# Kernel tuning notes

Hardware: AMD Instinct MI355X
Metric: run time of the kernel (lower is better)

The kernel has to match this reference:

```python
import jax, jax.numpy as jnp
import numpy as np

NUM_LEAVES = 256
EPS = 1e-6
SHARPNESS = 1.0   # init_sharpness, non-trainable buffer
BIAS_SHIFT = -2.0


def _generalized_gcd(w1, w2, lambd):
    # lambd: per-node bias -> andness via sigmoid; broadcast over batch
    lam = jax.nn.sigmoid(lambd)
    a = jnp.abs(w1) + EPS
    b = jnp.abs(w2) + EPS
    return lam * jnp.minimum(a, b) + (1.0 - lam) * jnp.maximum(a, b)


def setup_inputs() -> dict:
    key = jax.random.key(0)
    ks = jax.random.split(key, 6)
    B, L = 65536, NUM_LEAVES
    x = jax.random.normal(ks[0], (B, L), jnp.float32)
    # xavier-like scale for the leaf projection
    W_leaf = jax.random.normal(ks[1], (L, L), jnp.float32) * (1.0 / np.sqrt(L))
    weights = jax.random.uniform(ks[2], (L - 1, 2), jnp.float32, 0.5, 1.5)
    biases = jax.random.uniform(ks[3], (L - 1,), jnp.float32) * 0.1
    w_out = jax.random.normal(ks[4], (1, 1), jnp.float32)
    b_out = jnp.full((1,), 0.5, jnp.float32)
    return {"x": x, "W_leaf": W_leaf, "weights": weights,
            "biases": biases, "w_out": w_out, "b_out": b_out}


def reference(x, W_leaf, weights, biases, w_out, b_out):
    # InputToLeafFC: sigmoid(sharpness * (x @ W^T + bias_shift))
    leaf = jax.nn.sigmoid(SHARPNESS * (x @ W_leaf.T + BIAS_SHIFT))  # (B, L)

    # The original pops two nodes from the front of the queue and appends the
    # result; for a power-of-two leaf count this is exactly a level-by-level
    # pairwise tree reduction, with node weights consumed in order.
    cur = leaf
    off = 0
    n = cur.shape[1]
    while n > 1:  # log2(L) levels, each fully vectorized over (batch, pairs)
        m = n // 2
        w = weights[off:off + m]   # (m, 2)
        b = biases[off:off + m]    # (m,)
        left = cur[:, 0::2] * w[:, 0]
        right = cur[:, 1::2] * w[:, 1]
        cur = _generalized_gcd(left, right, b)  # (B, m)
        off += m
        n = m
    # fc_out: Linear(1,1) then sigmoid -> (B, 1)
    return jax.nn.sigmoid(cur * w_out[0, 0] + b_out[0])
```

## Files before the change

### kernel.cpp

```cpp
#include <hip/hip_runtime.h>
#include <stdint.h>


#define EPS 1e-6f
#define LOG2E 1.44269504088896340736f
#define WSTR 264
#define WIMG_SHORTS (256 * WSTR)
#define PARAM_OFF_B (WIMG_SHORTS * 2)

typedef __attribute__((ext_vector_type(8))) short short8;
typedef __attribute__((ext_vector_type(4))) short short4_t;
typedef __attribute__((ext_vector_type(4))) float float4_t;

__device__ __forceinline__ float fast_sigmoid(float z) {
    float e = __builtin_amdgcn_exp2f(-z * LOG2E);
    return __builtin_amdgcn_rcpf(1.0f + e);
}

__device__ __forceinline__ short f2bf(float f) {
    uint32_t u = __builtin_bit_cast(uint32_t, f);
    u += 0x7FFFu + ((u >> 16) & 1u);
    return (short)(u >> 16);
}

__device__ __forceinline__ float ggcd(float l, float r, float lam) {
    float a = fabsf(l) + EPS;
    float b = fabsf(r) + EPS;
    float mn = fminf(a, b);
    float mx = fmaxf(a, b);
    return fmaf(lam, mn - mx, mx);
}

__global__ __launch_bounds__(256)
void convert_w_kernel(const float* __restrict__ Wl,
                      const float* __restrict__ wts, const float* __restrict__ bia,
                      short* __restrict__ img) {
    int t = blockIdx.x * 256 + threadIdx.x;
    int j   = t >> 6;
    int kc4 = t & 63;
    const float4* Wv4 = (const float4*)Wl;
    float4 w4 = Wv4[j * 64 + kc4];
    int p = ((j & 15) << 4) | (j >> 4);
    short4_t s4;
    s4.x = f2bf(w4.x); s4.y = f2bf(w4.y); s4.z = f2bf(w4.z); s4.w = f2bf(w4.w);
    *(short4_t*)&img[p * WSTR + kc4 * 4] = s4;

    if (blockIdx.x == 0) {
        float4* pv = (float4*)((char*)img + PARAM_OFF_B);
        if (threadIdx.x < 255) {
            int n = threadIdx.x;
            pv[n] = make_float4(wts[2 * n], wts[2 * n + 1], fast_sigmoid(bia[n]), 0.f);
        } else if (threadIdx.x == 255) {
            pv[255] = make_float4(0.f, 0.f, 0.f, 0.f);
        }
    }
}

__global__ __launch_bounds__(1024, 4)
void btln_main(const float* __restrict__ x, const short* __restrict__ img,
               const float* __restrict__ wout, const float* __restrict__ bout,
               float* __restrict__ out) {
    __shared__ short Ws[WIMG_SHORTS];
    __shared__ float4 pv[256];

    const int tid  = threadIdx.x;
    const int lane = tid & 63;
    const int wv   = tid >> 6;
    const int c0   = lane & 15;
    const int q    = lane >> 4;

    {
        const uint4* img4 = (const uint4*)img;
        uint4* ws4 = (uint4*)Ws;
        const int n16 = (WIMG_SHORTS * 2) / 16;
        #pragma unroll
        for (int it = 0; it < 9; ++it) {
            int i = it * 1024 + tid;
            if (i < n16) ws4[i] = img4[i];
        }
        if (tid < 256) {
            const float4* gpv = (const float4*)((const char*)img + PARAM_OFF_B);
            pv[tid] = gpv[tid];
        }
    }
    __syncthreads();

    const int group   = blockIdx.x * 16 + wv;
    const int rowbase = group * 16;
    const float4* xv  = (const float4*)(x + (size_t)(rowbase + c0) * 256);

    float4_t acc[16];
    #pragma unroll
    for (int t = 0; t < 16; ++t) acc[t] = (float4_t){0.f, 0.f, 0.f, 0.f};

    float4 a0 = xv[q * 2];
    float4 a1 = xv[q * 2 + 1];
    #pragma unroll 1
    for (int kt = 0; kt < 8; ++kt) {
        const int ktn = (kt < 7) ? kt + 1 : 7;
        float4 b0 = xv[ktn * 8 + q * 2];
        float4 b1 = xv[ktn * 8 + q * 2 + 1];

        short8 af;
        af[0] = f2bf(a0.x); af[1] = f2bf(a0.y); af[2] = f2bf(a0.z); af[3] = f2bf(a0.w);
        af[4] = f2bf(a1.x); af[5] = f2bf(a1.y); af[6] = f2bf(a1.z); af[7] = f2bf(a1.w);

        const int kk = kt * 32;
        #pragma unroll
        for (int t = 0; t < 16; ++t) {
            short8 bf = *(const short8*)&Ws[(t * 16 + c0) * WSTR + kk + q * 8];
            acc[t] = __builtin_amdgcn_mfma_f32_16x16x32_bf16(af, bf, acc[t], 0, 0, 0);
        }
        a0 = b0; a1 = b1;
    }

    #pragma unroll
    for (int t = 0; t < 16; ++t) {
        #pragma unroll
        for (int r = 0; r < 4; ++r) acc[t][r] = fast_sigmoid(acc[t][r] - 2.0f);
    }
    #pragma unroll
    for (int tp = 0; tp < 8; ++tp) {
        float4 p = pv[c0 * 8 + tp];
        #pragma unroll
        for (int r = 0; r < 4; ++r)
            acc[tp][r] = ggcd(acc[2*tp][r] * p.x, acc[2*tp+1][r] * p.y, p.z);
    }
    #pragma unroll
    for (int tp = 0; tp < 4; ++tp) {
        float4 p = pv[128 + c0 * 4 + tp];
        #pragma unroll
        for (int r = 0; r < 4; ++r)
            acc[tp][r] = ggcd(acc[2*tp][r] * p.x, acc[2*tp+1][r] * p.y, p.z);
    }
    #pragma unroll
    for (int tp = 0; tp < 2; ++tp) {
        float4 p = pv[192 + c0 * 2 + tp];
        #pragma unroll
        for (int r = 0; r < 4; ++r)
            acc[tp][r] = ggcd(acc[2*tp][r] * p.x, acc[2*tp+1][r] * p.y, p.z);
    }
    float res[4];
    {
        float4 p = pv[224 + c0];
        #pragma unroll
        for (int r = 0; r < 4; ++r)
            res[r] = ggcd(acc[0][r] * p.x, acc[1][r] * p.y, p.z);
    }

    const int offs[4] = {240, 248, 252, 254};
    #pragma unroll
    for (int k = 0; k < 4; ++k) {
        float4 p = pv[offs[k] + (c0 >> (k + 1))];
        bool isLeft = ((c0 >> k) & 1) == 0;
        #pragma unroll
        for (int r = 0; r < 4; ++r) {
            float other = __shfl_xor(res[r], 1 << k, 64);
            float lf = isLeft ? res[r] : other;
            float rt = isLeft ? other  : res[r];
            res[r] = ggcd(lf * p.x, rt * p.y, p.z);
        }
    }

    if (c0 == 0) {
        const float wo = wout[0];
        const float bo = bout[0];
        #pragma unroll
        for (int r = 0; r < 4; ++r)
            out[rowbase + q * 4 + r] = fast_sigmoid(fmaf(res[r], wo, bo));
    }
}

extern "C" void kernel_launch(void* const* d_in, const int* in_sizes, int n_in,
                              void* d_out, int out_size, void* d_ws, size_t ws_size,
                              hipStream_t stream) {
    const float* x   = (const float*)d_in[0];
    const float* Wl  = (const float*)d_in[1];
    const float* wts = (const float*)d_in[2];
    const float* bia = (const float*)d_in[3];
    const float* wo  = (const float*)d_in[4];
    const float* bo  = (const float*)d_in[5];
    float* out = (float*)d_out;
    short* img = (short*)d_ws;

    convert_w_kernel<<<dim3(64), dim3(256), 0, stream>>>(Wl, wts, bia, img);

    const int rows = out_size;
    dim3 grid(rows / 256), block(1024);
    btln_main<<<grid, block, 0, stream>>>(x, img, wo, bo, out);
}
```

Baseline: 115.4 us.

## Fuse weight conversion into main kernel and process two row tiles per wave

Removes the separate W/param conversion kernel: each block now converts the fp32 W_leaf to bf16 straight into shared memory and computes the sigmoid biases itself. Blocks shrink to 512 threads, and each wave handles 32 rows as two 16-row MFMA tiles that share every B-fragment LDS read. This saves one launch and halves LDS traffic per MFMA, at the cost of redundant per-block conversion of W, more accumulator registers (two sets of 16 float4), and possibly lower occupancy.

```diff
diff --git a/kernel.cpp b/kernel.cpp
--- a/kernel.cpp
+++ b/kernel.cpp
@@ -6,7 +6,6 @@
 #define LOG2E 1.44269504088896340736f
 #define WSTR 264
 #define WIMG_SHORTS (256 * WSTR)
-#define PARAM_OFF_B (WIMG_SHORTS * 2)
 
 typedef __attribute__((ext_vector_type(8))) short short8;
 typedef __attribute__((ext_vector_type(4))) short short4_t;
@@ -31,89 +30,8 @@
     return fmaf(lam, mn - mx, mx);
 }
 
-__global__ __launch_bounds__(256)
-void convert_w_kernel(const float* __restrict__ Wl,
-                      const float* __restrict__ wts, const float* __restrict__ bia,
-                      short* __restrict__ img) {
-    int t = blockIdx.x * 256 + threadIdx.x;
-    int j   = t >> 6;
-    int kc4 = t & 63;
-    const float4* Wv4 = (const float4*)Wl;
-    float4 w4 = Wv4[j * 64 + kc4];
-    int p = ((j & 15) << 4) | (j >> 4);
-    short4_t s4;
-    s4.x = f2bf(w4.x); s4.y = f2bf(w4.y); s4.z = f2bf(w4.z); s4.w = f2bf(w4.w);
-    *(short4_t*)&img[p * WSTR + kc4 * 4] = s4;
-
-    if (blockIdx.x == 0) {
-        float4* pv = (float4*)((char*)img + PARAM_OFF_B);
-        if (threadIdx.x < 255) {
-            int n = threadIdx.x;
-            pv[n] = make_float4(wts[2 * n], wts[2 * n + 1], fast_sigmoid(bia[n]), 0.f);
-        } else if (threadIdx.x == 255) {
-            pv[255] = make_float4(0.f, 0.f, 0.f, 0.f);
-        }
-    }
-}
-
-__global__ __launch_bounds__(1024, 4)
-void btln_main(const float* __restrict__ x, const short* __restrict__ img,
-               const float* __restrict__ wout, const float* __restrict__ bout,
-               float* __restrict__ out) {
-    __shared__ short Ws[WIMG_SHORTS];
-    __shared__ float4 pv[256];
-
-    const int tid  = threadIdx.x;
-    const int lane = tid & 63;
-    const int wv   = tid >> 6;
-    const int c0   = lane & 15;
-    const int q    = lane >> 4;
-
-    {
-        const uint4* img4 = (const uint4*)img;
-        uint4* ws4 = (uint4*)Ws;
-        const int n16 = (WIMG_SHORTS * 2) / 16;
-        #pragma unroll
-        for (int it = 0; it < 9; ++it) {
-            int i = it * 1024 + tid;
-            if (i < n16) ws4[i] = img4[i];
-        }
-        if (tid < 256) {
-            const float4* gpv = (const float4*)((const char*)img + PARAM_OFF_B);
-            pv[tid] = gpv[tid];
-        }
-    }
-    __syncthreads();
-
-    const int group   = blockIdx.x * 16 + wv;
-    const int rowbase = group * 16;
-    const float4* xv  = (const float4*)(x + (size_t)(rowbase + c0) * 256);
-
-    float4_t acc[16];
-    #pragma unroll
-    for (int t = 0; t < 16; ++t) acc[t] = (float4_t){0.f, 0.f, 0.f, 0.f};
-
-    float4 a0 = xv[q * 2];
-    float4 a1 = xv[q * 2 + 1];
-    #pragma unroll 1
-    for (int kt = 0; kt < 8; ++kt) {
-        const int ktn = (kt < 7) ? kt + 1 : 7;
-        float4 b0 = xv[ktn * 8 + q * 2];
-        float4 b1 = xv[ktn * 8 + q * 2 + 1];
-
-        short8 af;
-        af[0] = f2bf(a0.x); af[1] = f2bf(a0.y); af[2] = f2bf(a0.z); af[3] = f2bf(a0.w);
-        af[4] = f2bf(a1.x); af[5] = f2bf(a1.y); af[6] = f2bf(a1.z); af[7] = f2bf(a1.w);
-
-        const int kk = kt * 32;
-        #pragma unroll
-        for (int t = 0; t < 16; ++t) {
-            short8 bf = *(const short8*)&Ws[(t * 16 + c0) * WSTR + kk + q * 8];
-            acc[t] = __builtin_amdgcn_mfma_f32_16x16x32_bf16(af, bf, acc[t], 0, 0, 0);
-        }
-        a0 = b0; a1 = b1;
-    }
-
+__device__ __forceinline__ void tree_reduce(float4_t acc[16], int c0,
+                                            const float4* pv, float res[4]) {
     #pragma unroll
     for (int t = 0; t < 16; ++t) {
         #pragma unroll
@@ -140,13 +58,84 @@
         for (int r = 0; r < 4; ++r)
             acc[tp][r] = ggcd(acc[2*tp][r] * p.x, acc[2*tp+1][r] * p.y, p.z);
     }
-    float res[4];
     {
         float4 p = pv[224 + c0];
         #pragma unroll
         for (int r = 0; r < 4; ++r)
             res[r] = ggcd(acc[0][r] * p.x, acc[1][r] * p.y, p.z);
     }
+}
+
+__global__ __launch_bounds__(512, 2)
+void btln_fused(const float* __restrict__ x, const float* __restrict__ Wl,
+                const float* __restrict__ wts, const float* __restrict__ bia,
+                const float* __restrict__ wout, const float* __restrict__ bout,
+                float* __restrict__ out) {
+    __shared__ short Ws[WIMG_SHORTS];
+    __shared__ float4 pv[256];
+
+    const int tid  = threadIdx.x;
+    const int lane = tid & 63;
+    const int wv   = tid >> 6;
+    const int c0   = lane & 15;
+    const int q    = lane >> 4;
+
+    {
+        const float4* Wv4 = (const float4*)Wl;
+        #pragma unroll 4
+        for (int it = 0; it < 32; ++it) {
+            int i   = it * 512 + tid;
+            int j   = i >> 6;
+            int kc4 = i & 63;
+            float4 w4 = Wv4[i];
+            int p = ((j & 15) << 4) | (j >> 4);
+            short4_t s4;
+            s4.x = f2bf(w4.x); s4.y = f2bf(w4.y); s4.z = f2bf(w4.z); s4.w = f2bf(w4.w);
+            *(short4_t*)&Ws[p * WSTR + kc4 * 4] = s4;
+        }
+    }
+    if (tid < 255)
+        pv[tid] = make_float4(wts[2 * tid], wts[2 * tid + 1], fast_sigmoid(bia[tid]), 0.f);
+    __syncthreads();
+
+    const int rowbase = blockIdx.x * 256 + wv * 32;
+    const float4* xv0 = (const float4*)(x + (size_t)(rowbase + c0) * 256);
+    const float4* xv1 = (const float4*)(x + (size_t)(rowbase + 16 + c0) * 256);
+
+    float4_t acc0[16], acc1[16];
+    #pragma unroll
+    for (int t = 0; t < 16; ++t) {
+        acc0[t] = (float4_t){0.f, 0.f, 0.f, 0.f};
+        acc1[t] = (float4_t){0.f, 0.f, 0.f, 0.f};
+    }
+
+    float4 a00 = xv0[q * 2], a01 = xv0[q * 2 + 1];
+    float4 a10 = xv1[q * 2], a11 = xv1[q * 2 + 1];
+    #pragma unroll 1
+    for (int kt = 0; kt < 8; ++kt) {
+        const int ktn = (kt < 7) ? kt + 1 : 7;
+        float4 n00 = xv0[ktn * 8 + q * 2], n01 = xv0[ktn * 8 + q * 2 + 1];
+        float4 n10 = xv1[ktn * 8 + q * 2], n11 = xv1[ktn * 8 + q * 2 + 1];
+
+        short8 af0, af1;
+        af0[0] = f2bf(a00.x); af0[1] = f2bf(a00.y); af0[2] = f2bf(a00.z); af0[3] = f2bf(a00.w);
+        af0[4] = f2bf(a01.x); af0[5] = f2bf(a01.y); af0[6] = f2bf(a01.z); af0[7] = f2bf(a01.w);
+        af1[0] = f2bf(a10.x); af1[1] = f2bf(a10.y); af1[2] = f2bf(a10.z); af1[3] = f2bf(a10.w);
+        af1[4] = f2bf(a11.x); af1[5] = f2bf(a11.y); af1[6] = f2bf(a11.z); af1[7] = f2bf(a11.w);
+
+        const int kk = kt * 32;
+        #pragma unroll
+        for (int t = 0; t < 16; ++t) {
+            short8 bf = *(const short8*)&Ws[(t * 16 + c0) * WSTR + kk + q * 8];
+            acc0[t] = __builtin_amdgcn_mfma_f32_16x16x32_bf16(af0, bf, acc0[t], 0, 0, 0);
+            acc1[t] = __builtin_amdgcn_mfma_f32_16x16x32_bf16(af1, bf, acc1[t], 0, 0, 0);
+        }
+        a00 = n00; a01 = n01; a10 = n10; a11 = n11;
+    }
+
+    float res0[4], res1[4];
+    tree_reduce(acc0, c0, pv, res0);
+    tree_reduce(acc1, c0, pv, res1);
 
     const int offs[4] = {240, 248, 252, 254};
     #pragma unroll
@@ -155,10 +144,12 @@
         bool isLeft = ((c0 >> k) & 1) == 0;
         #pragma unroll
         for (int r = 0; r < 4; ++r) {
-            float other = __shfl_xor(res[r], 1 << k, 64);
-            float lf = isLeft ? res[r] : other;
-            float rt = isLeft ? other  : res[r];
-            res[r] = ggcd(lf * p.x, rt * p.y, p.z);
+            float o0 = __shfl_xor(res0[r], 1 << k, 64);
+            float o1 = __shfl_xor(res1[r], 1 << k, 64);
+            float lf0 = isLeft ? res0[r] : o0, rt0 = isLeft ? o0 : res0[r];
+            float lf1 = isLeft ? res1[r] : o1, rt1 = isLeft ? o1 : res1[r];
+            res0[r] = ggcd(lf0 * p.x, rt0 * p.y, p.z);
+            res1[r] = ggcd(lf1 * p.x, rt1 * p.y, p.z);
         }
     }
 
@@ -166,8 +157,10 @@
         const float wo = wout[0];
         const float bo = bout[0];
         #pragma unroll
-        for (int r = 0; r < 4; ++r)
-            out[rowbase + q * 4 + r] = fast_sigmoid(fmaf(res[r], wo, bo));
+        for (int r = 0; r < 4; ++r) {
+            out[rowbase + q * 4 + r]      = fast_sigmoid(fmaf(res0[r], wo, bo));
+            out[rowbase + 16 + q * 4 + r] = fast_sigmoid(fmaf(res1[r], wo, bo));
+        }
     }
 }
 
@@ -181,11 +174,8 @@
     const float* wo  = (const float*)d_in[4];
     const float* bo  = (const float*)d_in[5];
     float* out = (float*)d_out;
-    short* img = (short*)d_ws;
-
-    convert_w_kernel<<<dim3(64), dim3(256), 0, stream>>>(Wl, wts, bia, img);
 
     const int rows = out_size;
-    dim3 grid(rows / 256), block(1024);
-    btln_main<<<grid, block, 0, stream>>>(x, img, wo, bo, out);
+    dim3 grid(rows / 256), block(512);
+    btln_fused<<<grid, block, 0, stream>>>(x, Wl, wts, bia, wo, bo, out);
 }
```

New measurement: 115.7 us. About the same (+0.3%).

## Stream swizzled bf16 weight tiles into double-buffered LDS via async global_load_lds

Applied to the files above, without the earlier changes.

The up-front copy of the full padded 135KB weight image into LDS is replaced by a K-tiled, XOR-swizzled weight layout. Each 64-wide K slab is streamed into a double-buffered 64KB LDS region with direct global-to-LDS loads, overlapped with the MFMA work on the previous slab. Blocks shrink to 512 threads and 128 rows to cut LDS use per block and allow more resident blocks. The cost is a barrier per K step and more blocks each re-reading the weight image from L2.

```diff
diff --git a/kernel.cpp b/kernel.cpp
--- a/kernel.cpp
+++ b/kernel.cpp
@@ -4,9 +4,7 @@
 
 #define EPS 1e-6f
 #define LOG2E 1.44269504088896340736f
-#define WSTR 264
-#define WIMG_SHORTS (256 * WSTR)
-#define PARAM_OFF_B (WIMG_SHORTS * 2)
+#define PARAM_OFF 131072
 
 typedef __attribute__((ext_vector_type(8))) short short8;
 typedef __attribute__((ext_vector_type(4))) short short4_t;
@@ -21,6 +19,13 @@
     uint32_t u = __builtin_bit_cast(uint32_t, f);
     u += 0x7FFFu + ((u >> 16) & 1u);
     return (short)(u >> 16);
+}
+
+__device__ __forceinline__ short8 pack8(float4 a, float4 b) {
+    short8 s;
+    s[0] = f2bf(a.x); s[1] = f2bf(a.y); s[2] = f2bf(a.z); s[3] = f2bf(a.w);
+    s[4] = f2bf(b.x); s[5] = f2bf(b.y); s[6] = f2bf(b.z); s[7] = f2bf(b.w);
+    return s;
 }
 
 __device__ __forceinline__ float ggcd(float l, float r, float lam) {
@@ -31,36 +36,80 @@
     return fmaf(lam, mn - mx, mx);
 }
 
+__device__ __forceinline__ void lds16(const void* g, void* l) {
+    __builtin_amdgcn_global_load_lds(
+        (const __attribute__((address_space(1))) unsigned int*)g,
+        (__attribute__((address_space(3))) unsigned int*)l, 16, 0, 0);
+}
+
+__device__ __forceinline__ void tree_reduce(float4_t acc[16], int c0,
+                                            const float4* pv, float res[4]) {
+    #pragma unroll
+    for (int t = 0; t < 16; ++t) {
+        #pragma unroll
+        for (int r = 0; r < 4; ++r) acc[t][r] = fast_sigmoid(acc[t][r] - 2.0f);
+    }
+    #pragma unroll
+    for (int tp = 0; tp < 8; ++tp) {
+        float4 p = pv[c0 * 8 + tp];
+        #pragma unroll
+        for (int r = 0; r < 4; ++r)
+            acc[tp][r] = ggcd(acc[2*tp][r] * p.x, acc[2*tp+1][r] * p.y, p.z);
+    }
+    #pragma unroll
+    for (int tp = 0; tp < 4; ++tp) {
+        float4 p = pv[128 + c0 * 4 + tp];
+        #pragma unroll
+        for (int r = 0; r < 4; ++r)
+            acc[tp][r] = ggcd(acc[2*tp][r] * p.x, acc[2*tp+1][r] * p.y, p.z);
+    }
+    #pragma unroll
+    for (int tp = 0; tp < 2; ++tp) {
+        float4 p = pv[192 + c0 * 2 + tp];
+        #pragma unroll
+        for (int r = 0; r < 4; ++r)
+            acc[tp][r] = ggcd(acc[2*tp][r] * p.x, acc[2*tp+1][r] * p.y, p.z);
+    }
+    {
+        float4 p = pv[224 + c0];
+        #pragma unroll
+        for (int r = 0; r < 4; ++r)
+            res[r] = ggcd(acc[0][r] * p.x, acc[1][r] * p.y, p.z);
+    }
+}
+
 __global__ __launch_bounds__(256)
-void convert_w_kernel(const float* __restrict__ Wl,
-                      const float* __restrict__ wts, const float* __restrict__ bia,
-                      short* __restrict__ img) {
-    int t = blockIdx.x * 256 + threadIdx.x;
-    int j   = t >> 6;
-    int kc4 = t & 63;
-    const float4* Wv4 = (const float4*)Wl;
-    float4 w4 = Wv4[j * 64 + kc4];
-    int p = ((j & 15) << 4) | (j >> 4);
+void convert_w(const float* __restrict__ Wl, const float* __restrict__ wts,
+               const float* __restrict__ bia, char* __restrict__ img) {
+    int i = blockIdx.x * 256 + threadIdx.x;
+    int a = i * 8;
+    int kt   = a >> 15;
+    int s    = a & 32767;
+    int j    = s >> 7;
+    int b    = s & 127;
+    int cpos = b >> 4;
+    int h    = (b >> 3) & 1;
+    int c    = cpos ^ (j & 7);
+    int k    = kt * 64 + c * 8 + h * 4;
+    int src  = ((j & 15) << 4) | (j >> 4);
+    float4 w4 = *(const float4*)&Wl[src * 256 + k];
     short4_t s4;
     s4.x = f2bf(w4.x); s4.y = f2bf(w4.y); s4.z = f2bf(w4.z); s4.w = f2bf(w4.w);
-    *(short4_t*)&img[p * WSTR + kc4 * 4] = s4;
-
-    if (blockIdx.x == 0) {
-        float4* pv = (float4*)((char*)img + PARAM_OFF_B);
-        if (threadIdx.x < 255) {
-            int n = threadIdx.x;
-            pv[n] = make_float4(wts[2 * n], wts[2 * n + 1], fast_sigmoid(bia[n]), 0.f);
-        } else if (threadIdx.x == 255) {
-            pv[255] = make_float4(0.f, 0.f, 0.f, 0.f);
-        }
-    }
-}
-
-__global__ __launch_bounds__(1024, 4)
-void btln_main(const float* __restrict__ x, const short* __restrict__ img,
+    *(short4_t*)&img[a] = s4;
+
+    if (i < 255) {
+        float4* pv = (float4*)(img + PARAM_OFF);
+        pv[i] = make_float4(wts[2 * i], wts[2 * i + 1], fast_sigmoid(bia[i]), 0.f);
+    } else if (i == 255) {
+        ((float4*)(img + PARAM_OFF))[255] = make_float4(0.f, 0.f, 0.f, 0.f);
+    }
+}
+
+__global__ __launch_bounds__(512, 4)
+void btln_main(const float* __restrict__ x, const char* __restrict__ img,
                const float* __restrict__ wout, const float* __restrict__ bout,
                float* __restrict__ out) {
-    __shared__ short Ws[WIMG_SHORTS];
+    __shared__ short Wt[2][16384];
     __shared__ float4 pv[256];
 
     const int tid  = threadIdx.x;
@@ -69,84 +118,63 @@
     const int c0   = lane & 15;
     const int q    = lane >> 4;
 
+    if (tid < 256) pv[tid] = ((const float4*)(img + PARAM_OFF))[tid];
+
     {
-        const uint4* img4 = (const uint4*)img;
-        uint4* ws4 = (uint4*)Ws;
-        const int n16 = (WIMG_SHORTS * 2) / 16;
-        #pragma unroll
-        for (int it = 0; it < 9; ++it) {
-            int i = it * 1024 + tid;
-            if (i < n16) ws4[i] = img4[i];
+        const char* g = img + wv * 4096 + lane * 16;
+        char* l = (char*)&Wt[0][wv * 2048];
+        #pragma unroll
+        for (int it = 0; it < 4; ++it)
+            lds16(g + it * 1024, l + it * 1024);
+    }
+
+    const int rowbase = blockIdx.x * 128 + wv * 16;
+    const float* xr = x + (size_t)(rowbase + c0) * 256;
+
+    float4_t acc[16];
+    #pragma unroll
+    for (int t = 0; t < 16; ++t) acc[t] = (float4_t){0.f, 0.f, 0.f, 0.f};
+
+    float4 a0 = *(const float4*)(xr + q * 8);
+    float4 a1 = *(const float4*)(xr + q * 8 + 4);
+    float4 a2 = *(const float4*)(xr + 32 + q * 8);
+    float4 a3 = *(const float4*)(xr + 32 + q * 8 + 4);
+
+    __syncthreads();
+
+    const int vx = c0 & 7;
+    #pragma unroll 1
+    for (int kt = 0; kt < 4; ++kt) {
+        const short* cur = Wt[kt & 1];
+        if (kt < 3) {
+            const char* g = img + (kt + 1) * 32768 + wv * 4096 + lane * 16;
+            char* l = (char*)&Wt[(kt + 1) & 1][wv * 2048];
+            #pragma unroll
+            for (int it = 0; it < 4; ++it)
+                lds16(g + it * 1024, l + it * 1024);
         }
-        if (tid < 256) {
-            const float4* gpv = (const float4*)((const char*)img + PARAM_OFF_B);
-            pv[tid] = gpv[tid];
+        const int kn = (kt < 3 ? kt + 1 : 3) * 64;
+        float4 b0 = *(const float4*)(xr + kn + q * 8);
+        float4 b1 = *(const float4*)(xr + kn + q * 8 + 4);
+        float4 b2 = *(const float4*)(xr + kn + 32 + q * 8);
+        float4 b3 = *(const float4*)(xr + kn + 32 + q * 8 + 4);
+
+        short8 af0 = pack8(a0, a1);
+        short8 af1 = pack8(a2, a3);
+        #pragma unroll
+        for (int t = 0; t < 16; ++t) {
+            const short* base = &cur[(t * 16 + c0) * 64];
+            short8 bf0 = *(const short8*)&base[(q ^ vx) * 8];
+            short8 bf1 = *(const short8*)&base[((q + 4) ^ vx) * 8];
+            acc[t] = __builtin_amdgcn_mfma_f32_16x16x32_bf16(af0, bf0, acc[t], 0, 0, 0);
+            acc[t] = __builtin_amdgcn_mfma_f32_16x16x32_bf16(af1, bf1, acc[t], 0, 0, 0);
         }
-    }
-    __syncthreads();
-
-    const int group   = blockIdx.x * 16 + wv;
-    const int rowbase = group * 16;
-    const float4* xv  = (const float4*)(x + (size_t)(rowbase + c0) * 256);
-
-    float4_t acc[16];
-    #pragma unroll
-    for (int t = 0; t < 16; ++t) acc[t] = (float4_t){0.f, 0.f, 0.f, 0.f};
-
-    float4 a0 = xv[q * 2];
-    float4 a1 = xv[q * 2 + 1];
-    #pragma unroll 1
-    for (int kt = 0; kt < 8; ++kt) {
-        const int ktn = (kt < 7) ? kt + 1 : 7;
-        float4 b0 = xv[ktn * 8 + q * 2];
-        float4 b1 = xv[ktn * 8 + q * 2 + 1];
-
-        short8 af;
-        af[0] = f2bf(a0.x); af[1] = f2bf(a0.y); af[2] = f2bf(a0.z); af[3] = f2bf(a0.w);
-        af[4] = f2bf(a1.x); af[5] = f2bf(a1.y); af[6] = f2bf(a1.z); af[7] = f2bf(a1.w);
-
-        const int kk = kt * 32;
-        #pragma unroll
-        for (int t = 0; t < 16; ++t) {
-            short8 bf = *(const short8*)&Ws[(t * 16 + c0) * WSTR + kk + q * 8];
-            acc[t] = __builtin_amdgcn_mfma_f32_16x16x32_bf16(af, bf, acc[t], 0, 0, 0);
-        }
-        a0 = b0; a1 = b1;
-    }
-
-    #pragma unroll
-    for (int t = 0; t < 16; ++t) {
-        #pragma unroll
-        for (int r = 0; r < 4; ++r) acc[t][r] = fast_sigmoid(acc[t][r] - 2.0f);
-    }
-    #pragma unroll
-    for (int tp = 0; tp < 8; ++tp) {
-        float4 p = pv[c0 * 8 + tp];
-        #pragma unroll
-        for (int r = 0; r < 4; ++r)
-            acc[tp][r] = ggcd(acc[2*tp][r] * p.x, acc[2*tp+1][r] * p.y, p.z);
-    }
-    #pragma unroll
-    for (int tp = 0; tp < 4; ++tp) {
-        float4 p = pv[128 + c0 * 4 + tp];
-        #pragma unroll
-        for (int r = 0; r < 4; ++r)
-            acc[tp][r] = ggcd(acc[2*tp][r] * p.x, acc[2*tp+1][r] * p.y, p.z);
-    }
-    #pragma unroll
-    for (int tp = 0; tp < 2; ++tp) {
-        float4 p = pv[192 + c0 * 2 + tp];
-        #pragma unroll
-        for (int r = 0; r < 4; ++r)
-            acc[tp][r] = ggcd(acc[2*tp][r] * p.x, acc[2*tp+1][r] * p.y, p.z);
-    }
+        __syncthreads();
+        a0 = b0; a1 = b1; a2 = b2; a3 = b3;
+    }
+
     float res[4];
-    {
-        float4 p = pv[224 + c0];
-        #pragma unroll
-        for (int r = 0; r < 4; ++r)
-            res[r] = ggcd(acc[0][r] * p.x, acc[1][r] * p.y, p.z);
-    }
+    tree_reduce(acc, c0, pv, res);
 
     const int offs[4] = {240, 248, 252, 254};
     #pragma unroll
@@ -181,11 +209,11 @@
     const float* wo  = (const float*)d_in[4];
     const float* bo  = (const float*)d_in[5];
     float* out = (float*)d_out;
-    short* img = (short*)d_ws;
-
-    convert_w_kernel<<<dim3(64), dim3(256), 0, stream>>>(Wl, wts, bia, img);
+    char* img = (char*)d_ws;
+
+    convert_w<<<dim3(64), dim3(256), 0, stream>>>(Wl, wts, bia, img);
 
     const int rows = out_size;
-    dim3 grid(rows / 256), block(1024);
+    dim3 grid(rows / 128), block(512);
     btln_main<<<grid, block, 0, stream>>>(x, img, wo, bo, out);
 }
```

After: 113.7 us. No clear change (-1.4%).
